# Kernel tuning notes

Hardware: AMD Instinct MI355X
Metric: run time of the kernel (lower is better)

The kernel has to match this reference:

```python
import jax, jax.numpy as jnp
import numpy as np

B, N, C_IN, L, C_OUT = 8, 50000, 32, 9, 64
M, NNZ = 12500, 37500


def setup_inputs() -> dict:
    key = jax.random.key(0)
    k = jax.random.split(key, 7)
    x = jax.random.normal(k[0], (B, N, C_IN), dtype=jnp.float32)
    weight = jax.random.normal(k[1], (L * C_IN, C_OUT), dtype=jnp.float32) * (1.0 / np.sqrt(L * C_IN))
    bias = jax.random.normal(k[2], (C_OUT,), dtype=jnp.float32) * 0.01
    values = jax.random.uniform(k[3], (NNZ,), dtype=jnp.float32)
    spiral_indices = jax.random.randint(k[4], (N, L), 0, N, dtype=jnp.int64)
    rows = jax.random.randint(k[5], (NNZ,), 0, M, dtype=jnp.int64)
    cols = jax.random.randint(k[6], (NNZ,), 0, N, dtype=jnp.int64)
    return {"x": x, "weight": weight, "bias": bias, "values": values,
            "spiral_indices": spiral_indices, "rows": rows, "cols": cols,
            "num_out_verts": M}


def reference(x, weight, bias, values, spiral_indices, rows, cols, num_out_verts):
    b, n, c = x.shape
    # SpiralConv: gather spiral neighborhoods, flatten, linear
    g = x[:, spiral_indices]                      # [B, N, L, C]
    g = g.reshape(b, n, -1)                       # [B, N, L*C]
    out = jnp.einsum('bnk,ko->bno', g, weight) + bias
    out = jax.nn.elu(out)                         # [B, N, C_OUT]
    # Pool: sparse down_transform (gather, scale, scatter_add)
    gathered = out[:, cols] * values[None, :, None]          # [B, NNZ, C_OUT]
    pooled = jnp.zeros((b, num_out_verts, out.shape[-1]), dtype=out.dtype)
    pooled = pooled.at[:, rows].add(gathered)                # [B, M, C_OUT]
    return pooled
```

## Files before the change

### kernel.cpp

```cpp
#include <hip/hip_runtime.h>
#include <hip/hip_bf16.h>

#define BATCH   8
#define NVERT   50000
#define CIN     32
#define LSP     9
#define COUT    64
#define MVERT   12500
#define NNZ     37500

#define TILE_T  64
#define TPB     586
#define NFRAG   2304
#define XELEMS  (BATCH * NVERT * CIN)
#define OUTDW   (BATCH * MVERT * COUT)

#define PRE_BLOCKS  6250
#define PACK_BLOCKS 9
#define ZERO_BLOCKS 6250

typedef __attribute__((ext_vector_type(8))) short  short8;
typedef __attribute__((ext_vector_type(4))) float  floatx4;

static __device__ __forceinline__ unsigned short f2bf(float f) {
    union { float f; unsigned int u; } c; c.f = f;
    unsigned int u = c.u;
    return (unsigned short)((u + 0x7fffu + ((u >> 16) & 1u)) >> 16);
}

static __device__ __forceinline__ void dma16(const void* g, void* l) {
    typedef __attribute__((address_space(1))) const void gvoid;
    typedef __attribute__((address_space(3))) void lvoid;
    __builtin_amdgcn_global_load_lds(
        (gvoid*)(unsigned long long)g,
        (lvoid*)(unsigned int)(unsigned long long)l,
        16, 0, 0);
}

__global__ __launch_bounds__(256)
void prep_kernel(const float* __restrict__ x, const float* __restrict__ w,
                 unsigned short* __restrict__ x16, unsigned short* __restrict__ wp,
                 float* __restrict__ out)
{
    const int blk = blockIdx.x;
    const int tid = threadIdx.x;
    if (blk < PRE_BLOCKS) {
        const size_t base = ((size_t)blk * 256 + tid) * 8;
        const float4* s = (const float4*)(x + base);
        float4 a = s[0], c = s[1];
        unsigned short t[8];
        t[0]=f2bf(a.x); t[1]=f2bf(a.y); t[2]=f2bf(a.z); t[3]=f2bf(a.w);
        t[4]=f2bf(c.x); t[5]=f2bf(c.y); t[6]=f2bf(c.z); t[7]=f2bf(c.w);
        *(uint4*)(x16 + base) = *(uint4*)t;
    } else if (blk < PRE_BLOCKS + PACK_BLOCKS) {
        const int f = (blk - PRE_BLOCKS) * 256 + tid;
        if (f < NFRAG) {
            int s = f >> 8, g = (f >> 6) & 3, lane = f & 63;
            int k0 = s * 32 + (lane >> 4) * 8, col = g * 16 + (lane & 15);
            unsigned short t[8];
            #pragma unroll
            for (int j = 0; j < 8; ++j)
                t[j] = f2bf(w[(size_t)(k0 + j) * COUT + col]);
            ((uint4*)wp)[f] = *(uint4*)t;
        }
    } else {
        const size_t base = ((size_t)(blk - PRE_BLOCKS - PACK_BLOCKS) * 256 + tid) * 4;
        if (base < OUTDW) *(uint4*)(out + base) = (uint4){0, 0, 0, 0};
    }
}

__global__ __launch_bounds__(256)
void spiral_mfma2_kernel(const unsigned short* __restrict__ x16,
                         const unsigned short* __restrict__ wp,
                         const float* __restrict__ bias,
                         const float* __restrict__ vals,
                         const int* __restrict__ spiral,
                         const int* __restrict__ rows,
                         const int* __restrict__ cols,
                         float* __restrict__ out)
{
    __shared__ unsigned short sG[NFRAG * 8];

    const int bid  = blockIdx.x;
    const int b    = bid / TPB;
    const int tile = bid - b * TPB;
    const int z0   = tile * TILE_T;
    const int tcnt = min(TILE_T, NNZ - z0);
    const int tid  = threadIdx.x;
    const int w    = tid >> 6;
    const int lane = tid & 63;

    int zc = z0 + lane; if (zc >= NNZ) zc = NNZ - 1;
    const int  c  = cols[zc];
    const int* sp = spiral + c * LSP;
    int idx[9];
    #pragma unroll
    for (int j = 0; j < 9; ++j) idx[j] = sp[j];

    const unsigned short* xb = x16 + (size_t)b * NVERT * CIN;
    #pragma unroll
    for (int j = 0; j < 9; ++j) {
        const unsigned short* src = xb + (size_t)idx[j] * CIN + w * 8;
        dma16(src, sG + (size_t)(4 * j + w) * 512);
    }
    __syncthreads();

    const int quad = lane >> 4;
    const int m16  = lane & 15;

    floatx4 acc[4];
    #pragma unroll
    for (int g = 0; g < 4; ++g) acc[g] = (floatx4){0.f, 0.f, 0.f, 0.f};

    #pragma unroll
    for (int s = 0; s < 9; ++s) {
        short8 af = *(const short8*)(sG + (size_t)((s * 4 + quad) * 64 + 16 * w + m16) * 8);
        #pragma unroll
        for (int g = 0; g < 4; ++g) {
            short8 bf = *(const short8*)(wp + (size_t)((s * 4 + g) * 64 + lane) * 8);
            acc[g] = __builtin_amdgcn_mfma_f32_16x16x32_bf16(af, bf, acc[g], 0, 0, 0);
        }
    }

    #pragma unroll
    for (int r = 0; r < 4; ++r) {
        int t = 16 * w + quad * 4 + r;
        if (t < tcnt) {
            int z   = z0 + t;
            float v = vals[z];
            int row = rows[z];
            float* dst = out + ((size_t)b * MVERT + row) * COUT;
            #pragma unroll
            for (int g = 0; g < 4; ++g) {
                int ch  = g * 16 + m16;
                float y = acc[g][r] + bias[ch];
                y = (y > 0.0f) ? y : (__expf(y) - 1.0f);
                atomicAdd(dst + ch, y * v);
            }
        }
    }
}

extern "C" void kernel_launch(void* const* d_in, const int* in_sizes, int n_in,
                              void* d_out, int out_size, void* d_ws, size_t ws_size,
                              hipStream_t stream) {
    const float* x      = (const float*)d_in[0];
    const float* w      = (const float*)d_in[1];
    const float* bias   = (const float*)d_in[2];
    const float* vals   = (const float*)d_in[3];
    const int*   spiral = (const int*)d_in[4];
    const int*   rows   = (const int*)d_in[5];
    const int*   cols   = (const int*)d_in[6];
    float* out = (float*)d_out;

    unsigned short* wp  = (unsigned short*)d_ws;
    unsigned short* x16 = (unsigned short*)((char*)d_ws + (size_t)NFRAG * 16);

    const int prep_grid = PRE_BLOCKS + PACK_BLOCKS + ZERO_BLOCKS;
    prep_kernel<<<prep_grid, 256, 0, stream>>>(x, w, x16, wp, out);
    spiral_mfma2_kernel<<<BATCH * TPB, 256, 0, stream>>>(x16, wp, bias, vals,
                                                         spiral, rows, cols, out);
}
```

Measured before the change: 211.2 us.

## Sort nonzeros by output row and pre-reduce runs before atomic adds

Adds histogram, scan and scatter kernels that bucket the sparse pooling entries by output row, so each tile handles row-sorted nonzeros. Within each wave, scaled ELU outputs are staged in shared memory and runs that share a row are summed before one atomicAdd per run, which cuts global atomic traffic. Gather staging is also made per-wave and waits on vmcnt instead of a block barrier. The cost is three extra small launches, including a single-block scan, on every call. With about three nonzeros per row, the runs are short, so the saving in atomics may be modest.

```diff
diff --git a/kernel.cpp b/kernel.cpp
--- a/kernel.cpp
+++ b/kernel.cpp
@@ -1,5 +1,4 @@
 #include <hip/hip_runtime.h>
-#include <hip/hip_bf16.h>
 
 #define BATCH   8
 #define NVERT   50000
@@ -12,12 +11,13 @@
 #define TILE_T  64
 #define TPB     586
 #define NFRAG   2304
+#define OUTDW   (BATCH * MVERT * COUT)
 #define XELEMS  (BATCH * NVERT * CIN)
-#define OUTDW   (BATCH * MVERT * COUT)
 
 #define PRE_BLOCKS  6250
 #define PACK_BLOCKS 9
 #define ZERO_BLOCKS 6250
+#define HZ_BLOCKS   49
 
 typedef __attribute__((ext_vector_type(8))) short  short8;
 typedef __attribute__((ext_vector_type(4))) float  floatx4;
@@ -40,7 +40,7 @@
 __global__ __launch_bounds__(256)
 void prep_kernel(const float* __restrict__ x, const float* __restrict__ w,
                  unsigned short* __restrict__ x16, unsigned short* __restrict__ wp,
-                 float* __restrict__ out)
+                 float* __restrict__ out, int* __restrict__ hist)
 {
     const int blk = blockIdx.x;
     const int tid = threadIdx.x;
@@ -63,23 +63,76 @@
                 t[j] = f2bf(w[(size_t)(k0 + j) * COUT + col]);
             ((uint4*)wp)[f] = *(uint4*)t;
         }
-    } else {
+    } else if (blk < PRE_BLOCKS + PACK_BLOCKS + ZERO_BLOCKS) {
         const size_t base = ((size_t)(blk - PRE_BLOCKS - PACK_BLOCKS) * 256 + tid) * 4;
         if (base < OUTDW) *(uint4*)(out + base) = (uint4){0, 0, 0, 0};
-    }
-}
-
-__global__ __launch_bounds__(256)
-void spiral_mfma2_kernel(const unsigned short* __restrict__ x16,
+    } else {
+        const int i = (blk - PRE_BLOCKS - PACK_BLOCKS - ZERO_BLOCKS) * 256 + tid;
+        if (i < MVERT) hist[i] = 0;
+    }
+}
+
+__global__ __launch_bounds__(256)
+void hist_kernel(const int* __restrict__ rows, int* __restrict__ hist) {
+    int z = blockIdx.x * 256 + threadIdx.x;
+    if (z < NNZ) atomicAdd(&hist[rows[z]], 1);
+}
+
+__global__ __launch_bounds__(1024)
+void scan_kernel(const int* __restrict__ hist, int* __restrict__ off2) {
+    __shared__ int sh[1024];
+    const int t = threadIdx.x;
+    const int base = t * 13;
+    int loc[13];
+    int s = 0;
+    #pragma unroll
+    for (int j = 0; j < 13; ++j) {
+        int i = base + j;
+        int v = (i < MVERT) ? hist[i] : 0;
+        loc[j] = s; s += v;
+    }
+    sh[t] = s;
+    __syncthreads();
+    for (int d = 1; d < 1024; d <<= 1) {
+        int v = (t >= d) ? sh[t - d] : 0;
+        __syncthreads();
+        sh[t] += v;
+        __syncthreads();
+    }
+    const int excl = sh[t] - s;
+    #pragma unroll
+    for (int j = 0; j < 13; ++j) {
+        int i = base + j;
+        if (i < MVERT) off2[i] = excl + loc[j];
+    }
+}
+
+__global__ __launch_bounds__(256)
+void scatter_kernel(const int* __restrict__ rows, const int* __restrict__ cols,
+                    const float* __restrict__ vals, int* __restrict__ off2,
+                    int* __restrict__ rows_s, int* __restrict__ cols_s,
+                    float* __restrict__ vals_s) {
+    int z = blockIdx.x * 256 + threadIdx.x;
+    if (z < NNZ) {
+        int r = rows[z];
+        int pos = atomicAdd(&off2[r], 1);
+        rows_s[pos] = r;
+        cols_s[pos] = cols[z];
+        vals_s[pos] = vals[z];
+    }
+}
+
+__global__ __launch_bounds__(256)
+void spiral_mfma3_kernel(const unsigned short* __restrict__ x16,
                          const unsigned short* __restrict__ wp,
                          const float* __restrict__ bias,
-                         const float* __restrict__ vals,
                          const int* __restrict__ spiral,
-                         const int* __restrict__ rows,
-                         const int* __restrict__ cols,
+                         const int* __restrict__ rows_s,
+                         const int* __restrict__ cols_s,
+                         const float* __restrict__ vals_s,
                          float* __restrict__ out)
 {
-    __shared__ unsigned short sG[NFRAG * 8];
+    __shared__ unsigned short sG[4 * 4608];
 
     const int bid  = blockIdx.x;
     const int b    = bid / TPB;
@@ -89,24 +142,26 @@
     const int tid  = threadIdx.x;
     const int w    = tid >> 6;
     const int lane = tid & 63;
-
-    int zc = z0 + lane; if (zc >= NNZ) zc = NNZ - 1;
-    const int  c  = cols[zc];
-    const int* sp = spiral + c * LSP;
-    int idx[9];
-    #pragma unroll
-    for (int j = 0; j < 9; ++j) idx[j] = sp[j];
-
-    const unsigned short* xb = x16 + (size_t)b * NVERT * CIN;
-    #pragma unroll
-    for (int j = 0; j < 9; ++j) {
-        const unsigned short* src = xb + (size_t)idx[j] * CIN + w * 8;
-        dma16(src, sG + (size_t)(4 * j + w) * 512);
-    }
-    __syncthreads();
-
     const int quad = lane >> 4;
     const int m16  = lane & 15;
+    const int z0w  = z0 + 16 * w;
+    int nval = tcnt - 16 * w;
+    nval = (nval < 0) ? 0 : ((nval > 16) ? 16 : nval);
+
+    unsigned short* region = sG + w * 4608;
+
+    const int zc    = min(z0w + m16, NNZ - 1);
+    const int c     = cols_s[zc];
+    const int myrow = rows_s[zc];
+    const int* sp   = spiral + c * LSP;
+
+    const unsigned short* xb = x16 + (size_t)b * NVERT * CIN;
+    #pragma unroll
+    for (int s = 0; s < 9; ++s) {
+        int idx = sp[s];
+        dma16(xb + (size_t)idx * CIN + quad * 8, region + s * 512);
+    }
+    asm volatile("s_waitcnt vmcnt(0)" ::: "memory");
 
     floatx4 acc[4];
     #pragma unroll
@@ -114,7 +169,7 @@
 
     #pragma unroll
     for (int s = 0; s < 9; ++s) {
-        short8 af = *(const short8*)(sG + (size_t)((s * 4 + quad) * 64 + 16 * w + m16) * 8);
+        short8 af = *(const short8*)(region + s * 512 + quad * 128 + m16 * 8);
         #pragma unroll
         for (int g = 0; g < 4; ++g) {
             short8 bf = *(const short8*)(wp + (size_t)((s * 4 + g) * 64 + lane) * 8);
@@ -122,22 +177,37 @@
         }
     }
 
-    #pragma unroll
-    for (int r = 0; r < 4; ++r) {
-        int t = 16 * w + quad * 4 + r;
-        if (t < tcnt) {
-            int z   = z0 + t;
-            float v = vals[z];
-            int row = rows[z];
-            float* dst = out + ((size_t)b * MVERT + row) * COUT;
+    if (nval > 0) {
+        float bs[4];
+        #pragma unroll
+        for (int g = 0; g < 4; ++g) bs[g] = bias[g * 16 + m16];
+        float vr[4];
+        #pragma unroll
+        for (int r = 0; r < 4; ++r) vr[r] = vals_s[min(z0w + quad * 4 + r, NNZ - 1)];
+
+        #pragma unroll
+        for (int r = 0; r < 4; ++r) {
+            const int tt = quad * 4 + r;
             #pragma unroll
             for (int g = 0; g < 4; ++g) {
-                int ch  = g * 16 + m16;
-                float y = acc[g][r] + bias[ch];
+                float y = acc[g][r] + bs[g];
                 y = (y > 0.0f) ? y : (__expf(y) - 1.0f);
-                atomicAdd(dst + ch, y * v);
+                *(float*)((char*)region + tt * 256 + (g * 16 + m16) * 4) = y * vr[r];
             }
         }
+
+        const int ch = lane;
+        float a = 0.0f;
+        int cur = __shfl(myrow, 0, 16);
+        for (int t = 0; t < nval; ++t) {
+            int rt = __shfl(myrow, t, 16);
+            if (rt != cur) {
+                atomicAdd(out + ((size_t)b * MVERT + cur) * COUT + ch, a);
+                a = 0.0f; cur = rt;
+            }
+            a += *(const float*)((char*)region + t * 256 + ch * 4);
+        }
+        atomicAdd(out + ((size_t)b * MVERT + cur) * COUT + ch, a);
     }
 }
 
@@ -153,11 +223,21 @@
     const int*   cols   = (const int*)d_in[6];
     float* out = (float*)d_out;
 
-    unsigned short* wp  = (unsigned short*)d_ws;
-    unsigned short* x16 = (unsigned short*)((char*)d_ws + (size_t)NFRAG * 16);
-
-    const int prep_grid = PRE_BLOCKS + PACK_BLOCKS + ZERO_BLOCKS;
-    prep_kernel<<<prep_grid, 256, 0, stream>>>(x, w, x16, wp, out);
-    spiral_mfma2_kernel<<<BATCH * TPB, 256, 0, stream>>>(x16, wp, bias, vals,
-                                                         spiral, rows, cols, out);
-}
+    char* base = (char*)d_ws;
+    unsigned short* wp     = (unsigned short*)(base);
+    unsigned short* x16    = (unsigned short*)(base + 36864);
+    int*            hist   = (int*)(base + 25636864);
+    int*            off2   = (int*)(base + 25686864);
+    int*            rows_s = (int*)(base + 25736864);
+    int*            cols_s = (int*)(base + 25886880);
+    float*          vals_s = (float*)(base + 26036896);
+
+    const int prep_grid = PRE_BLOCKS + PACK_BLOCKS + ZERO_BLOCKS + HZ_BLOCKS;
+    prep_kernel<<<prep_grid, 256, 0, stream>>>(x, w, x16, wp, out, hist);
+    hist_kernel<<<147, 256, 0, stream>>>(rows, hist);
+    scan_kernel<<<1, 1024, 0, stream>>>(hist, off2);
+    scatter_kernel<<<147, 256, 0, stream>>>(rows, cols, vals, off2,
+                                            rows_s, cols_s, vals_s);
+    spiral_mfma3_kernel<<<BATCH * TPB, 256, 0, stream>>>(x16, wp, bias, spiral,
+                                                         rows_s, cols_s, vals_s, out);
+}
```

New measurement: 185.0 us. -12.4%, faster.
